# Kernel optimization log

Measured on AMD Instinct MI355X. Metric: run time of the kernel, lower is better.

Reference implementation:

```python
import jax, jax.numpy as jnp
import numpy as np

N_RAYS = 32768
N_SAMPLES = 1048576
HID = 64
STEP = 0.0005


def _mlp(x, W1, b1, W2, b2, W3, b3):
    h = jax.nn.relu(x @ W1 + b1)
    h = jax.nn.relu(h @ W2 + b2)
    return h @ W3 + b3


def setup_inputs() -> dict:
    key = jax.random.key(0)
    ks = jax.random.split(key, 12)
    rays_o = jax.random.normal(ks[0], (N_RAYS, 3), jnp.float32)
    rays_d = jax.random.normal(ks[1], (N_RAYS, 3), jnp.float32)
    rays_d = rays_d / jnp.linalg.norm(rays_d, axis=-1, keepdims=True)
    t_starts = jax.random.uniform(ks[2], (N_SAMPLES,), jnp.float32, 0.0, 1.5)
    t_ends = t_starts + STEP
    ray_indices = jnp.sort(jax.random.randint(ks[3], (N_SAMPLES,), 0, N_RAYS, jnp.int32))
    def lin(k, fin, fout):
        return jax.random.normal(k, (fin, fout), jnp.float32) / np.sqrt(fin)
    return {
        'rays_o': rays_o, 'rays_d': rays_d,
        't_starts': t_starts, 't_ends': t_ends,
        'ray_indices': ray_indices,
        'W_d1': lin(ks[4], 3, HID), 'b_d1': jnp.zeros((HID,), jnp.float32),
        'W_d2': lin(ks[5], HID, HID), 'b_d2': jnp.zeros((HID,), jnp.float32),
        'W_d3': lin(ks[6], HID, 1), 'b_d3': jnp.zeros((1,), jnp.float32),
        'W_r1': lin(ks[7], 3, HID), 'b_r1': jnp.zeros((HID,), jnp.float32),
        'W_r2': lin(ks[8], HID, HID), 'b_r2': jnp.zeros((HID,), jnp.float32),
        'W_r3': lin(ks[9], HID, 3), 'b_r3': jnp.zeros((3,), jnp.float32),
    }


def reference(rays_o, rays_d, t_starts, t_ends, ray_indices,
              W_d1, b_d1, W_d2, b_d2, W_d3, b_d3,
              W_r1, b_r1, W_r2, b_r2, W_r3, b_r3):
    n_rays = rays_o.shape[0]
    mid = (t_starts + t_ends) * 0.5                      # [S]
    # gather ray origins/dirs per sample, compute positions
    positions = rays_o[ray_indices] + rays_d[ray_indices] * mid[:, None]  # [S,3]
    # density query (NGP decoder stand-in), softplus activation like trunc_exp family
    sigmas = jax.nn.softplus(_mlp(positions, W_d1, b_d1, W_d2, b_d2, W_d3, b_d3))[:, 0]  # [S]
    # render_weight_from_density: segment-wise exclusive cumsum of sigma*dt
    sigma_dt = sigmas * (t_ends - t_starts)              # [S]
    excl_global = jnp.cumsum(sigma_dt) - sigma_dt        # global exclusive cumsum
    per_ray = jax.ops.segment_sum(sigma_dt, ray_indices, num_segments=n_rays)  # [R]
    ray_excl = jnp.cumsum(per_ray) - per_ray             # exclusive cumsum over rays
    within_excl = excl_global - ray_excl[ray_indices]    # exclusive within each ray
    trans = jnp.exp(-within_excl)                        # transmittance
    alphas = 1.0 - jnp.exp(-sigma_dt)
    weights = trans * alphas
    # accumulate_along_rays (scatter-sum over ray_indices)
    opacities = jax.ops.segment_sum(weights, ray_indices, num_segments=n_rays)[:, None]  # [R,1]
    distances = jax.ops.segment_sum(weights * mid, ray_indices, num_segments=n_rays)[:, None]
    # rgb query
    rgbs = jax.nn.sigmoid(_mlp(positions, W_r1, b_r1, W_r2, b_r2, W_r3, b_r3))  # [S,3]
    w_sg = jax.lax.stop_gradient(weights)
    colors = jax.ops.segment_sum(w_sg[:, None] * rgbs, ray_indices, num_segments=n_rays)  # [R,3]
    # eval-mode background composition (nerf.training == False branch)
    rest = jax.lax.stop_gradient(1.0 - opacities)
    distances = distances + 5.0 * rest
    colors = colors + 0.5 * rest
    return colors, distances, opacities
```

## Files before the change

kernel.cpp:

```cpp
#include <hip/hip_runtime.h>
#include <hip/hip_bf16.h>
#include <math.h>

#define N_RAYS   32768
#define N_SAMP   1048576
#define HID      64
#define ITERS    4
#define BLK_HALF 1024
#define BLK_A    (2*BLK_HALF)

typedef short bf8 __attribute__((ext_vector_type(8)));
typedef float f4  __attribute__((ext_vector_type(4)));

union BF8U { bf8 v; unsigned u[4]; };

static __device__ __forceinline__ unsigned bfbits(float x) {
    union { __bf16 h; unsigned short s; } c; c.h = (__bf16)x; return (unsigned)c.s;
}
static __device__ __forceinline__ unsigned pk2(float a, float b) {
#if __has_builtin(__builtin_amdgcn_cvt_pk_bf16_f32)
    return __builtin_bit_cast(unsigned, __builtin_amdgcn_cvt_pk_bf16_f32(a, b));
#else
    return bfbits(a) | (bfbits(b) << 16);
#endif
}
static __device__ __forceinline__ unsigned pk2r(float a, float b) {
    return pk2(fmaxf(a, 0.f), fmaxf(b, 0.f));
}
static __device__ __forceinline__ f4 mfma16(bf8 a, bf8 b, f4 c) {
    return __builtin_amdgcn_mfma_f32_16x16x32_bf16(a, b, c, 0, 0, 0);
}

#define FRAG_SLOTS 14
#define BIAS_SLOTS 5

__global__ __launch_bounds__(128) void prep_frags(
    const float* __restrict__ Wd1, const float* __restrict__ bd1,
    const float* __restrict__ Wd2, const float* __restrict__ bd2,
    const float* __restrict__ Wd3, const float* __restrict__ bd3,
    const float* __restrict__ Wr1, const float* __restrict__ br1,
    const float* __restrict__ Wr2, const float* __restrict__ br2,
    const float* __restrict__ Wr3, const float* __restrict__ br3,
    uint4* __restrict__ fragbuf, float4* __restrict__ biasbuf)
{
    const int tid  = threadIdx.x;
    if (tid >= 128) return;
    const int net  = tid >> 6;
    const int lane = tid & 63;
    const int q    = lane >> 4;
    const int n    = lane & 15;
    const int qn   = n >> 2, rn = n & 3;
    const int rt   = n & 3;

    const float* W1 = net ? Wr1 : Wd1;  const float* b1 = net ? br1 : bd1;
    const float* W2 = net ? Wr2 : Wd2;  const float* b2 = net ? br2 : bd2;
    const float* W3 = net ? Wr3 : Wd3;  const float* b3 = net ? br3 : bd3;
    const int    nc = net ? 3 : 1;
    const int    ch = net ? (rt < 3 ? rt : 2) : 0;

    uint4*  fb = fragbuf + net * (FRAG_SLOTS * 64);
    float4* bb = biasbuf + net * (BIAS_SLOTS * 64);

    for (int t = 0; t < 4; ++t) {
        const int row = 8*qn + 4*(t&1) + rn + 32*(t>>1);
        uint4 f;
        f.x = pk2(W1[row],       W1[HID+row]);
        f.y = pk2(W1[2*HID+row], b1[row]);
        f.z = 0u; f.w = 0u;
        fb[t*64 + lane] = f;
    }
    for (int t = 0; t < 4; ++t) {
        const int row = 8*qn + 4*(t&1) + rn + 32*(t>>1);
        for (int s = 0; s < 2; ++s) {
            unsigned u[4];
            for (int dw = 0; dw < 4; ++dw) {
                const int k = 8*q + 2*dw + 32*s;
                u[dw] = pk2(W2[k*HID+row], W2[(k+1)*HID+row]);
            }
            fb[(4 + 2*t + s)*64 + lane] = make_uint4(u[0], u[1], u[2], u[3]);
        }
    }
    for (int s = 0; s < 2; ++s) {
        unsigned u[4];
        for (int dw = 0; dw < 4; ++dw) {
            const int kg = 32*s + 8*q + 2*dw;
            u[dw] = pk2(W3[kg*nc + ch], W3[(kg+1)*nc + ch]);
        }
        fb[(12 + s)*64 + lane] = make_uint4(u[0], u[1], u[2], u[3]);
    }
    for (int t = 0; t < 4; ++t) {
        float4 f;
        f.x = b2[8*q + 4*(t&1) + 0 + 32*(t>>1)];
        f.y = b2[8*q + 4*(t&1) + 1 + 32*(t>>1)];
        f.z = b2[8*q + 4*(t&1) + 2 + 32*(t>>1)];
        f.w = b2[8*q + 4*(t&1) + 3 + 32*(t>>1)];
        bb[t*64 + lane] = f;
    }
    {
        float4 f;
        f.x = b3[0];
        f.y = net ? b3[1] : b3[0];
        f.z = net ? b3[2] : b3[0];
        f.w = net ? b3[2] : b3[0];
        bb[4*64 + lane] = f;
    }
}

__global__ __launch_bounds__(256, 3) void pass_a(
    const float* __restrict__ rays_o, const float* __restrict__ rays_d,
    const float* __restrict__ t_starts, const float* __restrict__ t_ends,
    const int*   __restrict__ ray_idx,
    const uint4* __restrict__ fragbuf, const float4* __restrict__ biasbuf,
    float4* __restrict__ ws4, float* __restrict__ ws_mid,
    int* __restrict__ start)
{
    const bool is_rgb = blockIdx.x >= BLK_HALF;
    const int  blk    = is_rgb ? (blockIdx.x - BLK_HALF) : blockIdx.x;
    const int  lane   = threadIdx.x & 63;
    const int  wv     = ((blk << 8) + threadIdx.x) >> 6;
    const int  q      = lane >> 4;

    const uint4*  fb = fragbuf + (is_rgb ? FRAG_SLOTS*64 : 0);
    const float4* bb = biasbuf + (is_rgb ? BIAS_SLOTS*64 : 0);

    bf8 a1[4];
    #pragma unroll
    for (int t = 0; t < 4; ++t)
        a1[t] = __builtin_bit_cast(bf8, fb[t*64 + lane]);
    bf8 a2[4][2];
    #pragma unroll
    for (int t = 0; t < 4; ++t)
        #pragma unroll
        for (int s = 0; s < 2; ++s)
            a2[t][s] = __builtin_bit_cast(bf8, fb[(4 + 2*t + s)*64 + lane]);
    bf8 a3[2];
    #pragma unroll
    for (int s = 0; s < 2; ++s)
        a3[s] = __builtin_bit_cast(bf8, fb[(12 + s)*64 + lane]);
    f4 bias2[4];
    #pragma unroll
    for (int t = 0; t < 4; ++t)
        bias2[t] = __builtin_bit_cast(f4, bb[t*64 + lane]);
    f4 bias3 = __builtin_bit_cast(f4, bb[4*64 + lane]);

    const int base0 = wv * (ITERS * 64);

    #pragma unroll 1
    for (int it = 0; it < ITERS; ++it) {
        const int smp = base0 + it * 64 + lane;

        const float ts = t_starts[smp], te = t_ends[smp];
        const int   ri = ray_idx[smp];
        const float mid = 0.5f*(ts+te), dt = te - ts;
        const float px = rays_o[3*ri+0] + rays_d[3*ri+0]*mid;
        const float py = rays_o[3*ri+1] + rays_d[3*ri+1]*mid;
        const float pz = rays_o[3*ri+2] + rays_d[3*ri+2]*mid;
        const unsigned p01 = pk2(px, py);
        const unsigned p23 = pk2(pz, 1.0f);

        if (!is_rgb) {
            int rp = __shfl_up(ri, 1, 64);
            if (lane == 0) rp = (smp == 0) ? -1 : ray_idx[smp-1];
            for (int rr = rp + 1; rr <= ri; ++rr) start[rr] = smp;
            if (smp == N_SAMP - 1)
                for (int rr = ri + 1; rr <= N_RAYS; ++rr) start[rr] = N_SAMP;
        }

        f4 mine = {0.f, 0.f, 0.f, 0.f};

        #pragma unroll
        for (int u = 0; u < 4; ++u) {
            BF8U xb;
            xb.u[0] = (q == u) ? p01 : 0u;
            xb.u[1] = (q == u) ? p23 : 0u;
            xb.u[2] = 0u; xb.u[3] = 0u;

            const f4 zero = {0.f, 0.f, 0.f, 0.f};
            f4 d1[4];
            #pragma unroll
            for (int t = 0; t < 4; ++t) d1[t] = mfma16(a1[t], xb.v, zero);

            bf8 bf2[2];
            #pragma unroll
            for (int s = 0; s < 2; ++s) {
                BF8U p;
                p.u[0] = pk2r(d1[2*s][0],   d1[2*s][1]);
                p.u[1] = pk2r(d1[2*s][2],   d1[2*s][3]);
                p.u[2] = pk2r(d1[2*s+1][0], d1[2*s+1][1]);
                p.u[3] = pk2r(d1[2*s+1][2], d1[2*s+1][3]);
                bf2[s] = p.v;
            }

            f4 d2[4];
            #pragma unroll
            for (int t = 0; t < 4; ++t) {
                f4 a = bias2[t];
                a = mfma16(a2[t][0], bf2[0], a);
                a = mfma16(a2[t][1], bf2[1], a);
                d2[t] = a;
            }

            bf8 bf3[2];
            #pragma unroll
            for (int s = 0; s < 2; ++s) {
                BF8U p;
                p.u[0] = pk2r(d2[2*s][0],   d2[2*s][1]);
                p.u[1] = pk2r(d2[2*s][2],   d2[2*s][3]);
                p.u[2] = pk2r(d2[2*s+1][0], d2[2*s+1][1]);
                p.u[3] = pk2r(d2[2*s+1][2], d2[2*s+1][3]);
                bf3[s] = p.v;
            }

            f4 c3 = bias3;
            c3 = mfma16(a3[0], bf3[0], c3);
            c3 = mfma16(a3[1], bf3[1], c3);

            if (q == u) mine = c3;
        }

        float* w4 = (float*)(ws4 + smp);
        if (!is_rgb) {
            const float sg = mine[0];
            const float sp = fmaxf(sg, 0.f) + __logf(1.f + __expf(-fabsf(sg)));
            w4[3] = sp * dt;
            ws_mid[smp] = mid;
        } else {
            w4[0] = __builtin_amdgcn_rcpf(1.f + __expf(-mine[0]));
            w4[1] = __builtin_amdgcn_rcpf(1.f + __expf(-mine[1]));
            w4[2] = __builtin_amdgcn_rcpf(1.f + __expf(-mine[2]));
        }
    }
}

__global__ __launch_bounds__(256) void pass_b(
    const float4* __restrict__ ws4, const float* __restrict__ ws_mid,
    const int* __restrict__ start, float* __restrict__ out)
{
    const int lane = threadIdx.x & 63;
    const int wv   = (blockIdx.x * blockDim.x + threadIdx.x) >> 6;
    const int half = lane >> 5;
    const int l32  = lane & 31;
    const int r    = 2*wv + half;
    if (r >= N_RAYS) return;

    int s0 = start[r], s1 = start[r+1];
    s0 = min(max(s0, 0), N_SAMP);
    s1 = min(max(s1, s0), N_SAMP);

    float cum = 0.f, opac = 0.f, dist = 0.f, c0 = 0.f, c1 = 0.f, c2 = 0.f;

    for (int base = s0; base < s1; base += 32) {
        int s = base + l32;
        bool ok = s < s1;
        float4 v  = ok ? ws4[s]    : make_float4(0.f, 0.f, 0.f, 0.f);
        float mid = ok ? ws_mid[s] : 0.f;
        float sd  = v.w;

        float x = sd;
        #pragma unroll
        for (int off = 1; off < 32; off <<= 1) {
            float y = __shfl_up(x, off, 32);
            if (l32 >= off) x += y;
        }
        float incl = cum + x;
        float excl = incl - sd;
        float w = __expf(-excl) - __expf(-incl);
        dist += w*mid; c0 += w*v.x; c1 += w*v.y; c2 += w*v.z;

        float tot = __shfl(x, 31, 32);
        opac += __expf(-cum) - __expf(-(cum + tot));
        cum  += tot;
    }

    #pragma unroll
    for (int off = 16; off > 0; off >>= 1) {
        dist += __shfl_xor(dist, off, 32);
        c0   += __shfl_xor(c0,   off, 32);
        c1   += __shfl_xor(c1,   off, 32);
        c2   += __shfl_xor(c2,   off, 32);
    }

    if (l32 == 0) {
        float rest = 1.f - opac;
        out[r*3 + 0] = c0 + 0.5f * rest;
        out[r*3 + 1] = c1 + 0.5f * rest;
        out[r*3 + 2] = c2 + 0.5f * rest;
        out[3*N_RAYS + r] = dist + 5.f * rest;
        out[4*N_RAYS + r] = opac;
    }
}

extern "C" void kernel_launch(void* const* d_in, const int* in_sizes, int n_in,
                              void* d_out, int out_size, void* d_ws, size_t ws_size,
                              hipStream_t stream) {
    const float* rays_o   = (const float*)d_in[0];
    const float* rays_d   = (const float*)d_in[1];
    const float* t_starts = (const float*)d_in[2];
    const float* t_ends   = (const float*)d_in[3];
    const int*   ray_idx  = (const int*)  d_in[4];
    const float* Wd1 = (const float*)d_in[5];  const float* bd1 = (const float*)d_in[6];
    const float* Wd2 = (const float*)d_in[7];  const float* bd2 = (const float*)d_in[8];
    const float* Wd3 = (const float*)d_in[9];  const float* bd3 = (const float*)d_in[10];
    const float* Wr1 = (const float*)d_in[11]; const float* br1 = (const float*)d_in[12];
    const float* Wr2 = (const float*)d_in[13]; const float* br2 = (const float*)d_in[14];
    const float* Wr3 = (const float*)d_in[15]; const float* br3 = (const float*)d_in[16];

    float4* ws4    = (float4*)d_ws;
    float*  ws_mid = (float*)(ws4 + N_SAMP);
    char*   p      = (char*)(ws_mid + N_SAMP);
    int*    startb  = (int*)p;
    uint4*  fragbuf = (uint4*)(p + (((N_RAYS+1)*4 + 255) & ~255));
    float4* biasbuf = (float4*)(fragbuf + 2*FRAG_SLOTS*64);
    float*  out     = (float*)d_out;

    hipLaunchKernelGGL(prep_frags, dim3(1), dim3(128), 0, stream,
                       Wd1, bd1, Wd2, bd2, Wd3, bd3,
                       Wr1, br1, Wr2, br2, Wr3, br3, fragbuf, biasbuf);

    hipLaunchKernelGGL(pass_a, dim3(BLK_A), dim3(256), 0, stream,
                       rays_o, rays_d, t_starts, t_ends, ray_idx,
                       fragbuf, biasbuf, ws4, ws_mid, startb);

    hipLaunchKernelGGL(pass_b, dim3((N_RAYS/2 * 64) / 256), dim3(256), 0, stream,
                       ws4, ws_mid, startb, out);
}
```

Before: 148.1 us.

## Cut pass_a registers for 4 waves/SIMD, use K16 MFMA for layer 1, parallelize prep

Raises pass_a's launch-bounds occupancy target from 3 to 4 blocks. To fit, it frees registers: the layer-2 biases are stored packed as bf16 pairs and unpacked per use, and the output biases come from scalar loads. The first layer now uses the 16x16x16 bf16 MFMA with 4-element fragments instead of zero-padded 16x16x32, which halves that layer's matrix work and fragment registers. prep_frags is split across 8 blocks with one job per wavefront instead of a single serial block. Rounding the layer-2 bias to bf16 adds precision error whenever the biases are nonzero.

```diff
diff --git a/kernel.cpp b/kernel.cpp
--- a/kernel.cpp
+++ b/kernel.cpp
@@ -10,9 +10,17 @@
 #define BLK_A    (2*BLK_HALF)
 
 typedef short bf8 __attribute__((ext_vector_type(8)));
+typedef short bf4 __attribute__((ext_vector_type(4)));
 typedef float f4  __attribute__((ext_vector_type(4)));
 
 union BF8U { bf8 v; unsigned u[4]; };
+union BF4U { bf4 v; unsigned u[2]; };
+
+#if __has_builtin(__builtin_amdgcn_mfma_f32_16x16x16bf16_1k)
+#define HAVE_M16 1
+#else
+#define HAVE_M16 0
+#endif
 
 static __device__ __forceinline__ unsigned bfbits(float x) {
     union { __bf16 h; unsigned short s; } c; c.h = (__bf16)x; return (unsigned)c.s;
@@ -30,11 +38,17 @@
 static __device__ __forceinline__ f4 mfma16(bf8 a, bf8 b, f4 c) {
     return __builtin_amdgcn_mfma_f32_16x16x32_bf16(a, b, c, 0, 0, 0);
 }
+static __device__ __forceinline__ float lo2f(unsigned u) {
+    return __builtin_bit_cast(float, u << 16);
+}
+static __device__ __forceinline__ float hi2f(unsigned u) {
+    return __builtin_bit_cast(float, u & 0xffff0000u);
+}
 
 #define FRAG_SLOTS 14
 #define BIAS_SLOTS 5
 
-__global__ __launch_bounds__(128) void prep_frags(
+__global__ __launch_bounds__(256) void prep_frags(
     const float* __restrict__ Wd1, const float* __restrict__ bd1,
     const float* __restrict__ Wd2, const float* __restrict__ bd2,
     const float* __restrict__ Wd3, const float* __restrict__ bd3,
@@ -43,10 +57,11 @@
     const float* __restrict__ Wr3, const float* __restrict__ br3,
     uint4* __restrict__ fragbuf, float4* __restrict__ biasbuf)
 {
-    const int tid  = threadIdx.x;
-    if (tid >= 128) return;
-    const int net  = tid >> 6;
-    const int lane = tid & 63;
+    const int g = blockIdx.x * blockDim.x + threadIdx.x;
+    if (g >= 2048) return;
+    const int net  = g >> 10;
+    const int job  = (g >> 6) & 15;
+    const int lane = g & 63;
     const int q    = lane >> 4;
     const int n    = lane & 15;
     const int qn   = n >> 2, rn = n & 3;
@@ -61,42 +76,42 @@
     uint4*  fb = fragbuf + net * (FRAG_SLOTS * 64);
     float4* bb = biasbuf + net * (BIAS_SLOTS * 64);
 
-    for (int t = 0; t < 4; ++t) {
+    if (job < 8) {
+        const int t = job >> 1, s = job & 1;
+        const int row = 8*qn + 4*(t&1) + rn + 32*(t>>1);
+        unsigned u[4];
+        #pragma unroll
+        for (int dw = 0; dw < 4; ++dw) {
+            const int k = 8*q + 2*dw + 32*s;
+            u[dw] = pk2(W2[k*HID+row], W2[(k+1)*HID+row]);
+        }
+        fb[(4 + job)*64 + lane] = make_uint4(u[0], u[1], u[2], u[3]);
+    } else if (job < 12) {
+        const int t = job - 8;
         const int row = 8*qn + 4*(t&1) + rn + 32*(t>>1);
         uint4 f;
         f.x = pk2(W1[row],       W1[HID+row]);
         f.y = pk2(W1[2*HID+row], b1[row]);
         f.z = 0u; f.w = 0u;
         fb[t*64 + lane] = f;
-    }
-    for (int t = 0; t < 4; ++t) {
-        const int row = 8*qn + 4*(t&1) + rn + 32*(t>>1);
-        for (int s = 0; s < 2; ++s) {
-            unsigned u[4];
-            for (int dw = 0; dw < 4; ++dw) {
-                const int k = 8*q + 2*dw + 32*s;
-                u[dw] = pk2(W2[k*HID+row], W2[(k+1)*HID+row]);
-            }
-            fb[(4 + 2*t + s)*64 + lane] = make_uint4(u[0], u[1], u[2], u[3]);
-        }
-    }
-    for (int s = 0; s < 2; ++s) {
+
+        const int base = 8*q + 4*(t&1) + 32*(t>>1);
+        float4 g4;
+        g4.x = b2[base + 0];
+        g4.y = b2[base + 1];
+        g4.z = b2[base + 2];
+        g4.w = b2[base + 3];
+        bb[t*64 + lane] = g4;
+    } else if (job < 14) {
+        const int s = job - 12;
         unsigned u[4];
+        #pragma unroll
         for (int dw = 0; dw < 4; ++dw) {
             const int kg = 32*s + 8*q + 2*dw;
             u[dw] = pk2(W3[kg*nc + ch], W3[(kg+1)*nc + ch]);
         }
         fb[(12 + s)*64 + lane] = make_uint4(u[0], u[1], u[2], u[3]);
-    }
-    for (int t = 0; t < 4; ++t) {
-        float4 f;
-        f.x = b2[8*q + 4*(t&1) + 0 + 32*(t>>1)];
-        f.y = b2[8*q + 4*(t&1) + 1 + 32*(t>>1)];
-        f.z = b2[8*q + 4*(t&1) + 2 + 32*(t>>1)];
-        f.w = b2[8*q + 4*(t&1) + 3 + 32*(t>>1)];
-        bb[t*64 + lane] = f;
-    }
-    {
+    } else if (job == 14) {
         float4 f;
         f.x = b3[0];
         f.y = net ? b3[1] : b3[0];
@@ -106,11 +121,12 @@
     }
 }
 
-__global__ __launch_bounds__(256, 3) void pass_a(
+__global__ __launch_bounds__(256, 4) void pass_a(
     const float* __restrict__ rays_o, const float* __restrict__ rays_d,
     const float* __restrict__ t_starts, const float* __restrict__ t_ends,
     const int*   __restrict__ ray_idx,
     const uint4* __restrict__ fragbuf, const float4* __restrict__ biasbuf,
+    const float* __restrict__ bd3, const float* __restrict__ br3,
     float4* __restrict__ ws4, float* __restrict__ ws_mid,
     int* __restrict__ start)
 {
@@ -123,10 +139,23 @@
     const uint4*  fb = fragbuf + (is_rgb ? FRAG_SLOTS*64 : 0);
     const float4* bb = biasbuf + (is_rgb ? BIAS_SLOTS*64 : 0);
 
+#if HAVE_M16
+    bf4 a1[4];
+    {
+        const uint2* fb2 = (const uint2*)fb;
+        #pragma unroll
+        for (int t = 0; t < 4; ++t) {
+            const uint2 w = fb2[(t*64 + lane)*2];
+            BF4U c; c.u[0] = w.x; c.u[1] = w.y;
+            a1[t] = c.v;
+        }
+    }
+#else
     bf8 a1[4];
     #pragma unroll
     for (int t = 0; t < 4; ++t)
         a1[t] = __builtin_bit_cast(bf8, fb[t*64 + lane]);
+#endif
     bf8 a2[4][2];
     #pragma unroll
     for (int t = 0; t < 4; ++t)
@@ -137,11 +166,18 @@
     #pragma unroll
     for (int s = 0; s < 2; ++s)
         a3[s] = __builtin_bit_cast(bf8, fb[(12 + s)*64 + lane]);
-    f4 bias2[4];
-    #pragma unroll
-    for (int t = 0; t < 4; ++t)
-        bias2[t] = __builtin_bit_cast(f4, bb[t*64 + lane]);
-    f4 bias3 = __builtin_bit_cast(f4, bb[4*64 + lane]);
+
+    unsigned b2p[8];
+    #pragma unroll
+    for (int t = 0; t < 4; ++t) {
+        const float4 b = bb[t*64 + lane];
+        b2p[2*t+0] = pk2(b.x, b.y);
+        b2p[2*t+1] = pk2(b.z, b.w);
+    }
+    const float* b3 = is_rgb ? br3 : bd3;
+    const float b30 = b3[0];
+    const float b31 = is_rgb ? b3[1] : b30;
+    const float b32 = is_rgb ? b3[2] : b30;
 
     const int base0 = wv * (ITERS * 64);
 
@@ -170,15 +206,23 @@
 
         #pragma unroll
         for (int u = 0; u < 4; ++u) {
+            const f4 zero = {0.f, 0.f, 0.f, 0.f};
+            f4 d1[4];
+#if HAVE_M16
+            BF4U xb;
+            xb.u[0] = (q == u) ? p01 : 0u;
+            xb.u[1] = (q == u) ? p23 : 0u;
+            #pragma unroll
+            for (int t = 0; t < 4; ++t)
+                d1[t] = __builtin_amdgcn_mfma_f32_16x16x16bf16_1k(a1[t], xb.v, zero, 0, 0, 0);
+#else
             BF8U xb;
             xb.u[0] = (q == u) ? p01 : 0u;
             xb.u[1] = (q == u) ? p23 : 0u;
             xb.u[2] = 0u; xb.u[3] = 0u;
-
-            const f4 zero = {0.f, 0.f, 0.f, 0.f};
-            f4 d1[4];
             #pragma unroll
             for (int t = 0; t < 4; ++t) d1[t] = mfma16(a1[t], xb.v, zero);
+#endif
 
             bf8 bf2[2];
             #pragma unroll
@@ -194,7 +238,9 @@
             f4 d2[4];
             #pragma unroll
             for (int t = 0; t < 4; ++t) {
-                f4 a = bias2[t];
+                f4 a;
+                a[0] = lo2f(b2p[2*t+0]); a[1] = hi2f(b2p[2*t+0]);
+                a[2] = lo2f(b2p[2*t+1]); a[3] = hi2f(b2p[2*t+1]);
                 a = mfma16(a2[t][0], bf2[0], a);
                 a = mfma16(a2[t][1], bf2[1], a);
                 d2[t] = a;
@@ -211,7 +257,7 @@
                 bf3[s] = p.v;
             }
 
-            f4 c3 = bias3;
+            f4 c3 = {b30, b31, b32, b32};
             c3 = mfma16(a3[0], bf3[0], c3);
             c3 = mfma16(a3[1], bf3[1], c3);
 
@@ -313,13 +359,13 @@
     float4* biasbuf = (float4*)(fragbuf + 2*FRAG_SLOTS*64);
     float*  out     = (float*)d_out;
 
-    hipLaunchKernelGGL(prep_frags, dim3(1), dim3(128), 0, stream,
+    hipLaunchKernelGGL(prep_frags, dim3(8), dim3(256), 0, stream,
                        Wd1, bd1, Wd2, bd2, Wd3, bd3,
                        Wr1, br1, Wr2, br2, Wr3, br3, fragbuf, biasbuf);
 
     hipLaunchKernelGGL(pass_a, dim3(BLK_A), dim3(256), 0, stream,
                        rays_o, rays_d, t_starts, t_ends, ray_idx,
-                       fragbuf, biasbuf, ws4, ws_mid, startb);
+                       fragbuf, biasbuf, bd3, br3, ws4, ws_mid, startb);
 
     hipLaunchKernelGGL(pass_b, dim3((N_RAYS/2 * 64) / 256), dim3(256), 0, stream,
                        ws4, ws_mid, startb, out);
```

New measurement: 148.1 us. No clear change (+0.0%).
